# Performance work log

Measured on AMD Instinct MI355X. Metric: run time of the kernel, lower is better.

## Reference

```python
import jax, jax.numpy as jnp
import numpy as np

N = 4096          # total ensemble boxes per frame
M = 20            # MAX_MERGE_NUMS
H = 16            # MergeNet hidden_c
COND_THRES = 0.2
IOU_THRES = 0.3


def setup_inputs() -> dict:
    key = jax.random.key(0)
    ks = jax.random.split(key, 6)
    u = jax.random.uniform(ks[0], (N, 9), dtype=jnp.float32)
    # realistic lidar boxes: centers in a ~140x80x8m range, dims in [0.5, 4.5), heading in [-pi, pi)
    centers = (u[:, 0:3] - 0.5) * jnp.array([140.0, 80.0, 8.0], jnp.float32)
    dims = u[:, 3:6] * 4.0 + 0.5
    heading = (u[:, 6:7] - 0.5) * (2.0 * np.pi)
    extra = u[:, 7:9]  # extra box attrs (cols 7:9), untouched by merge
    pred_boxes = jnp.concatenate([centers, dims, heading, extra], axis=-1)
    pred_scores = jax.random.uniform(ks[1], (N,), dtype=jnp.float32)
    pred_labels = jax.random.randint(ks[2], (N,), 0, 3)
    w1 = (jax.random.normal(ks[3], (M, H), jnp.float32) / np.sqrt(M)).astype(jnp.float32)
    b1 = jnp.zeros((H,), jnp.float32)
    w2 = (jax.random.normal(ks[4], (H, H), jnp.float32) / np.sqrt(H)).astype(jnp.float32)
    b2 = jnp.zeros((H,), jnp.float32)
    w3 = (jax.random.normal(ks[5], (H, 1), jnp.float32) / np.sqrt(H)).astype(jnp.float32)
    b3 = jnp.zeros((1,), jnp.float32)
    return dict(pred_boxes=pred_boxes, pred_scores=pred_scores, pred_labels=pred_labels,
                w1=w1, b1=b1, w2=w2, b2=b2, w3=w3, b3=b3)


def _bev_aligned(b):
    # boxes3d_lidar_to_aligned_bev_boxes: swap dx/dy when |limit_period(heading)| >= pi/4
    ang = b[..., 6] - jnp.floor(b[..., 6] / np.pi + 0.5) * np.pi
    swap = jnp.abs(ang) >= (np.pi / 4)
    dx = jnp.where(swap, b[..., 4], b[..., 3])
    dy = jnp.where(swap, b[..., 3], b[..., 4])
    return jnp.stack([b[..., 0] - dx / 2, b[..., 1] - dy / 2,
                      b[..., 0] + dx / 2, b[..., 1] + dy / 2], axis=-1)


def _iou_one_many(a, b):
    # axis-aligned BEV IoU of one box a[4] vs many b[N,4]
    xmin = jnp.maximum(a[0], b[:, 0]); ymin = jnp.maximum(a[1], b[:, 1])
    xmax = jnp.minimum(a[2], b[:, 2]); ymax = jnp.minimum(a[3], b[:, 3])
    inter = jnp.maximum(xmax - xmin, 0.0) * jnp.maximum(ymax - ymin, 0.0)
    area_a = (a[2] - a[0]) * (a[3] - a[1])
    area_b = (b[:, 2] - b[:, 0]) * (b[:, 3] - b[:, 1])
    return inter / jnp.maximum(area_a + area_b - inter, 1e-6)


def _nms_merge(pred_boxes, pred_scores, pred_labels, w1, b1, w2, b2, w3, b3):
    valid = pred_scores > COND_THRES
    sort_key = jnp.where(valid, pred_scores, -jnp.inf)
    order = jnp.argsort(-sort_key)                 # descending by score; invalid sink
    boxes9 = pred_boxes[order]
    labels = pred_labels[order]
    scores = pred_scores[order]
    suppressed0 = ~valid[order]
    boxes7 = boxes9[:, :7]
    bev0 = _bev_aligned(boxes7)                    # merged boxes get suppressed, so bev is static

    def mergenet(ob):                              # ob: [M, 7] -> merged box [7]
        x = ob.T                                   # [7, M] (k is the feature axis)
        h = jax.nn.relu(x @ w1 + b1)
        h = jax.nn.relu(h @ w2 + b2)
        return (h @ w3 + b3)[:, 0]

    def step(suppressed, i):
        active = ~suppressed[i]
        same = (labels == labels[i]) & (~suppressed)
        iou = _iou_one_many(bev0[i], bev0)         # [N]
        over = (iou > IOU_THRES) & same            # includes self (iou=1)
        count = jnp.sum(over)
        rank = jnp.cumsum(over) - 1                # slot of each overlap, in score order
        tgt = jnp.where(over & (rank < M), rank, M)
        ob = jnp.zeros((M, 7), boxes7.dtype).at[tgt].set(boxes7, mode='drop')
        bi = boxes7[i]
        new_box = jnp.where(count > 1, mergenet(ob), bi)
        new_box = new_box.at[3:6].set(jnp.maximum(new_box[3:6], 1e-5))
        out_box = jnp.where(active, new_box, bi)
        return suppressed | (over & active), (out_box, active)

    _, (merged7, keep) = jax.lax.scan(step, suppressed0, jnp.arange(N))
    out_boxes = jnp.concatenate([merged7, boxes9[:, 7:9]], axis=-1)   # [N, 9]
    return out_boxes, scores, labels, keep


def reference(pred_boxes, pred_scores, pred_labels, w1, b1, w2, b2, w3, b3):
    # Returns fixed-shape (boxes9, scores, labels, keep_mask); rows with keep=False
    # correspond to boxes that torch's dynamic version would have removed.
    return _nms_merge(pred_boxes, pred_scores, pred_labels, w1, b1, w2, b2, w3, b3)
```

## Files before the change

kernel.cpp:

```cpp
#include <hip/hip_runtime.h>
#include <cstdint>

typedef unsigned long long u64;
typedef unsigned int u32;

#define NB 4096
#define NW 64
#define MM 20
#define HH 16
#define COND_THRES 0.2f
#define IOU_THRES 0.3f
#define PI_F  3.14159265358979323846f
#define PI4_F 0.78539816339744830962f

#define WS_KEPT    0
#define WS_MASK    32768
#define WS_BOX9S   (WS_MASK + NB*NW*8)
#define WS_BEVS    (WS_BOX9S + NB*9*4)
#define WS_SCORES  (WS_BEVS + NB*16)
#define WS_LABELS  (WS_SCORES + NB*4)
#define WS_SUPSTEP (WS_LABELS + NB*4)
#define WS_NBRW    (WS_SUPSTEP + NB*4)
#define WS_PART    (WS_NBRW + NB*8)

__device__ __forceinline__ u64 sort_key(float s, int i) {
  u32 sb = (s > COND_THRES) ? __float_as_uint(s) : 0u;
  return ((u64)(sb ^ 0xFFFFFFFFu) << 12) | (u64)i;
}

__global__ void __launch_bounds__(256) k_rank(const float* __restrict__ scores,
                                              u32* __restrict__ partial,
                                              u64* __restrict__ nbrw) {
  __shared__ u64 kj[256];
  int tid = threadIdx.x;
  int j = blockIdx.y * 256 + tid;
  kj[tid] = sort_key(scores[j], j);
  __syncthreads();
  int i = blockIdx.x * 256 + tid;
  if (blockIdx.y == 0) nbrw[i] = 0;
  u64 ki = sort_key(scores[i], i);
  int cnt = 0;
  #pragma unroll 16
  for (int t = 0; t < 256; ++t) cnt += (kj[t] < ki) ? 1 : 0;
  partial[i * 16 + blockIdx.y] = (u32)cnt;
}

__global__ void __launch_bounds__(256) k_scatter(const u32* __restrict__ partial,
                                                 const float* __restrict__ scores,
                                                 const float* __restrict__ boxes9,
                                                 const int* __restrict__ labels,
                                                 float* __restrict__ box9s, float4* __restrict__ bevs,
                                                 float* __restrict__ scoress, int* __restrict__ labelss) {
  #pragma clang fp contract(off)
  int i = blockIdx.x * 256 + threadIdx.x;
  const uint4* p4 = (const uint4*)(partial + i * 16);
  uint4 a0 = p4[0], a1 = p4[1], a2 = p4[2], a3 = p4[3];
  int r = (int)(a0.x + a0.y + a0.z + a0.w + a1.x + a1.y + a1.z + a1.w +
                a2.x + a2.y + a2.z + a2.w + a3.x + a3.y + a3.z + a3.w);
  float b[9];
  #pragma unroll
  for (int f = 0; f < 9; ++f) b[f] = boxes9[i * 9 + f];
  #pragma unroll
  for (int f = 0; f < 9; ++f) box9s[r * 9 + f] = b[f];
  float ang = b[6] - floorf(b[6] / PI_F + 0.5f) * PI_F;
  bool sw = fabsf(ang) >= PI4_F;
  float dx = sw ? b[4] : b[3];
  float dy = sw ? b[3] : b[4];
  bevs[r] = make_float4(b[0] - dx * 0.5f, b[1] - dy * 0.5f,
                        b[0] + dx * 0.5f, b[1] + dy * 0.5f);
  scoress[r] = scores[i];
  labelss[r] = labels[i];
}

__global__ void __launch_bounds__(64) k_mask(const float4* __restrict__ bevs,
                                             const int* __restrict__ labelss,
                                             const float* __restrict__ scoress,
                                             u64* __restrict__ mask,
                                             u64* __restrict__ nbrw) {
  #pragma clang fp contract(off)
  __shared__ float4 bj[64];
  __shared__ int lj[64];
  int t = threadIdx.x;
  int jt = blockIdx.x;
  int it = blockIdx.y;
  int j = jt * 64 + t;
  bj[t] = bevs[j];
  lj[t] = labelss[j];
  u64 vj = __ballot(scoress[j] > COND_THRES);
  int i = it * 64 + t;
  float4 a = bevs[i];
  int la = labelss[i];
  float area_a = (a.z - a.x) * (a.w - a.y);
  __syncthreads();
  u64 w = 0;
  #pragma unroll 8
  for (int kk = 0; kk < 64; ++kk) {
    float4 bb = bj[kk];
    float xmin = fmaxf(a.x, bb.x), ymin = fmaxf(a.y, bb.y);
    float xmax = fminf(a.z, bb.z), ymax = fminf(a.w, bb.w);
    float inter = fmaxf(xmax - xmin, 0.0f) * fmaxf(ymax - ymin, 0.0f);
    float area_b = (bb.z - bb.x) * (bb.w - bb.y);
    float iou = inter / fmaxf(area_a + area_b - inter, 1e-6f);
    if ((iou > IOU_THRES) && (la == lj[kk])) w |= (1ull << kk);
  }
  mask[(u64)i * NW + jt] = w;
  if (jt <= it) {
    u64 below = (jt < it) ? ~0ull : ((1ull << t) - 1ull);
    if (w & vj & below) atomicOr(&nbrw[i], 1ull << jt);
  }
}

__global__ void __launch_bounds__(1024) k_nms(const u64* __restrict__ mask,
                                              const u64* __restrict__ nbrw,
                                              const float* __restrict__ scoress,
                                              u64* __restrict__ keptOut) {
  __shared__ u64 decided[64], kept[64];
  __shared__ int remaining;
  int tid = threadIdx.x;
  if (tid < 64) {
    u64 v = 0;
    #pragma unroll 8
    for (int b = 0; b < 64; ++b)
      if (scoress[(tid << 6) | b] > COND_THRES) v |= (1ull << b);
    decided[tid] = ~v;
    kept[tid] = 0;
  }
  if (tid == 0) remaining = 0;
  __syncthreads();
  if (tid < 64) atomicAdd(&remaining, __popcll(~decided[tid]));
  u64 cw0[4], cw1[4];
  u32 meta[4];
  #pragma unroll
  for (int s = 0; s < 4; ++s) {
    int i = tid + (s << 10);
    int wi = i >> 6;
    u64 bit = 1ull << (i & 63);
    u64 t = nbrw[i];
    int n = 0; u32 ovf = 0;
    u64 c0 = 0, c1 = 0; u32 i0 = 0, i1 = 0;
    while (t) {
      int w = __builtin_ctzll(t);
      t &= t - 1;
      u64 below = (w < wi) ? ~0ull : (bit - 1ull);
      u64 m = mask[(u64)i * NW + w] & below;
      if (n == 0)      { c0 = m; i0 = (u32)w; }
      else if (n == 1) { c1 = m; i1 = (u32)w; }
      else ovf = 1;
      ++n;
    }
    cw0[s] = c0; cw1[s] = c1;
    meta[s] = i0 | (i1 << 6) | ((u32)(n > 2 ? 2 : n) << 12) | (ovf << 14);
  }
  __syncthreads();
  while (remaining > 0) {
    int decIdx[4]; bool decKept[4]; int nDec = 0;
    #pragma unroll
    for (int s = 0; s < 4; ++s) {
      int i = tid + (s << 10);
      int wi = i >> 6;
      u64 bit = 1ull << (i & 63);
      if (decided[wi] & bit) continue;
      bool hasU = false, hasK = false;
      u32 mt = meta[s];
      if (!(mt & (1u << 14))) {
        int n = (mt >> 12) & 3;
        if (n >= 1) {
          int w = mt & 63;
          hasU = hasU || ((cw0[s] & ~decided[w]) != 0ull);
          hasK = hasK || ((cw0[s] & kept[w]) != 0ull);
        }
        if (n >= 2) {
          int w = (mt >> 6) & 63;
          hasU = hasU || ((cw1[s] & ~decided[w]) != 0ull);
          hasK = hasK || ((cw1[s] & kept[w]) != 0ull);
        }
      } else {
        u64 t = nbrw[i];
        while (t) {
          int w = __builtin_ctzll(t);
          t &= t - 1;
          u64 below = (w < wi) ? ~0ull : (bit - 1ull);
          u64 m = mask[(u64)i * NW + w] & below;
          hasU = hasU || ((m & ~decided[w]) != 0ull);
          hasK = hasK || ((m & kept[w]) != 0ull);
        }
      }
      if (!hasU) { decIdx[nDec] = i; decKept[nDec] = !hasK; ++nDec; }
    }
    __syncthreads();
    for (int d = 0; d < nDec; ++d) {
      int i = decIdx[d];
      u64 bit = 1ull << (i & 63);
      atomicOr(&decided[i >> 6], bit);
      if (decKept[d]) atomicOr(&kept[i >> 6], bit);
      atomicSub(&remaining, 1);
    }
    __syncthreads();
  }
  if (tid < 64) keptOut[tid] = kept[tid];
}

__global__ void __launch_bounds__(256) k_supstep(const u64* __restrict__ mask,
                                                 const u64* __restrict__ kept,
                                                 const float* __restrict__ scoress,
                                                 int* __restrict__ supstep) {
  __shared__ u64 K[64];
  if (threadIdx.x < 64) K[threadIdx.x] = kept[threadIdx.x];
  __syncthreads();
  int j = blockIdx.x * 256 + threadIdx.x;
  if (!(scoress[j] > COND_THRES)) { supstep[j] = -1; return; }
  int res = 0x7FFFFFFF;
  #pragma unroll 4
  for (int w = 0; w < 64; ++w) {
    u64 m = mask[(u64)j * NW + w] & K[w];
    if (m) { res = (w << 6) + __builtin_ctzll(m); break; }
  }
  supstep[j] = res;
}

__global__ void __launch_bounds__(64) k_merge(
    const u64* __restrict__ mask, const int* __restrict__ supstep,
    const float* __restrict__ box9s, const float* __restrict__ scoress,
    const int* __restrict__ labelss,
    const float* __restrict__ w1, const float* __restrict__ b1,
    const float* __restrict__ w2, const float* __restrict__ b2,
    const float* __restrict__ w3, const float* __restrict__ b3,
    float* __restrict__ out) {
  #pragma clang fp contract(off)
  __shared__ int candList[MM];
  __shared__ float ob[MM][7];
  __shared__ float h1[7][HH];
  __shared__ float h2[7][HH];
  __shared__ float res[7];
  int i = blockIdx.x;
  int t = threadIdx.x;
  bool active = (supstep[i] == i);
  u64 wq = 0;
  int cnt = 0;
  if (active) {
    u64 w = mask[(u64)i * NW + t];
    while (w) {
      int b = __builtin_ctzll(w);
      w &= w - 1;
      int j = (t << 6) | b;
      if (supstep[j] >= i) { wq |= (1ull << b); cnt++; }
    }
  }
  int incl = cnt;
  #pragma unroll
  for (int off = 1; off < 64; off <<= 1) {
    int v = __shfl_up(incl, off);
    if (t >= off) incl += v;
  }
  int excl = incl - cnt;
  int count = __shfl(incl, 63);
  bool merged = active && (count > 1);
  if (merged && wq) {
    int pos = excl;
    u64 ww = wq;
    while (ww && pos < MM) {
      int b = __builtin_ctzll(ww);
      ww &= ww - 1;
      candList[pos++] = (t << 6) | b;
    }
  }
  __syncthreads();
  if (merged) {
    int nc = count < MM ? count : MM;
    if (t < MM) {
      if (t < nc) {
        int j = candList[t];
        #pragma unroll
        for (int f = 0; f < 7; ++f) ob[t][f] = box9s[j * 9 + f];
      } else {
        #pragma unroll
        for (int f = 0; f < 7; ++f) ob[t][f] = 0.0f;
      }
    }
    __syncthreads();
    for (int o = t; o < 7 * HH; o += 64) {
      int f = o >> 4, hh = o & 15;
      float acc = b1[hh];
      #pragma unroll
      for (int m = 0; m < MM; ++m) acc += ob[m][f] * w1[m * HH + hh];
      h1[f][hh] = fmaxf(acc, 0.0f);
    }
    __syncthreads();
    for (int o = t; o < 7 * HH; o += 64) {
      int f = o >> 4, oo = o & 15;
      float acc = b2[oo];
      #pragma unroll
      for (int k = 0; k < HH; ++k) acc += h1[f][k] * w2[k * HH + oo];
      h2[f][oo] = fmaxf(acc, 0.0f);
    }
    __syncthreads();
    if (t < 7) {
      float acc = b3[0];
      #pragma unroll
      for (int k = 0; k < HH; ++k) acc += h2[t][k] * w3[k];
      if (t >= 3 && t < 6) acc = fmaxf(acc, 1e-5f);
      res[t] = acc;
    }
    __syncthreads();
  }
  if (t < 9) {
    float v = box9s[i * 9 + t];
    if (merged && t < 7) v = res[t];
    out[i * 9 + t] = v;
  }
  if (t == 0) {
    out[NB * 9 + i]          = scoress[i];
    out[NB * 9 + NB + i]     = (float)labelss[i];
    out[NB * 9 + 2 * NB + i] = active ? 1.0f : 0.0f;
  }
}

extern "C" void kernel_launch(void* const* d_in, const int* in_sizes, int n_in,
                              void* d_out, int out_size, void* d_ws, size_t ws_size,
                              hipStream_t stream) {
  const float* boxes9 = (const float*)d_in[0];
  const float* scores = (const float*)d_in[1];
  const int*   labels = (const int*)d_in[2];
  const float* w1 = (const float*)d_in[3];
  const float* b1 = (const float*)d_in[4];
  const float* w2 = (const float*)d_in[5];
  const float* b2 = (const float*)d_in[6];
  const float* w3 = (const float*)d_in[7];
  const float* b3 = (const float*)d_in[8];
  char* ws = (char*)d_ws;
  u64*    kept    = (u64*)(ws + WS_KEPT);
  u64*    mask    = (u64*)(ws + WS_MASK);
  float*  box9s   = (float*)(ws + WS_BOX9S);
  float4* bevs    = (float4*)(ws + WS_BEVS);
  float*  scoress = (float*)(ws + WS_SCORES);
  int*    labelss = (int*)(ws + WS_LABELS);
  int*    supstep = (int*)(ws + WS_SUPSTEP);
  u64*    nbrw    = (u64*)(ws + WS_NBRW);
  u32*    part    = (u32*)(ws + WS_PART);
  float*  out     = (float*)d_out;

  hipLaunchKernelGGL(k_rank,    dim3(16, 16),   dim3(256),  0, stream, scores, part, nbrw);
  hipLaunchKernelGGL(k_scatter, dim3(NB / 256), dim3(256),  0, stream, part, scores, boxes9, labels,
                     box9s, bevs, scoress, labelss);
  hipLaunchKernelGGL(k_mask,    dim3(64, 64),   dim3(64),   0, stream, bevs, labelss, scoress,
                     mask, nbrw);
  hipLaunchKernelGGL(k_nms,     dim3(1),        dim3(1024), 0, stream, mask, nbrw, scoress, kept);
  hipLaunchKernelGGL(k_supstep, dim3(NB / 256), dim3(256),  0, stream, mask, kept, scoress, supstep);
  hipLaunchKernelGGL(k_merge,   dim3(NB),       dim3(64),   0, stream, mask, supstep,
                     box9s, scoress, labelss, w1, b1, w2, b2, w3, b3, out);
}
```

Before: 132.7 us.

## Fuse rank and scatter kernels; drop supstep pass by recomputing suppression in merge

Merges the score-ranking and scatter kernels into one k_sort kernel. In it, each group of 16 threads counts one element's rank over all tiles, reduces the count with shuffles, and writes the sorted box data. This removes the partial-count buffer. The k_supstep kernel is also removed: k_merge now takes kept and valid bitmasks and, for each active box, checks whether each overlapping candidate is suppressed by an earlier kept box by scanning its mask rows. This saves two launches and intermediate round-trips, but adds a per-candidate scan of mask words inside k_merge that could be costly for late boxes.

```diff
diff --git a/kernel.cpp b/kernel.cpp
--- a/kernel.cpp
+++ b/kernel.cpp
@@ -14,62 +14,63 @@
 #define PI4_F 0.78539816339744830962f
 
 #define WS_KEPT    0
+#define WS_VALID   512
 #define WS_MASK    32768
 #define WS_BOX9S   (WS_MASK + NB*NW*8)
 #define WS_BEVS    (WS_BOX9S + NB*9*4)
 #define WS_SCORES  (WS_BEVS + NB*16)
 #define WS_LABELS  (WS_SCORES + NB*4)
-#define WS_SUPSTEP (WS_LABELS + NB*4)
-#define WS_NBRW    (WS_SUPSTEP + NB*4)
-#define WS_PART    (WS_NBRW + NB*8)
+#define WS_NBRW    (WS_LABELS + NB*4)
 
 __device__ __forceinline__ u64 sort_key(float s, int i) {
   u32 sb = (s > COND_THRES) ? __float_as_uint(s) : 0u;
   return ((u64)(sb ^ 0xFFFFFFFFu) << 12) | (u64)i;
 }
 
-__global__ void __launch_bounds__(256) k_rank(const float* __restrict__ scores,
-                                              u32* __restrict__ partial,
+__global__ void __launch_bounds__(256) k_sort(const float* __restrict__ scores,
+                                              const float* __restrict__ boxes9,
+                                              const int* __restrict__ labels,
+                                              float* __restrict__ box9s, float4* __restrict__ bevs,
+                                              float* __restrict__ scoress, int* __restrict__ labelss,
                                               u64* __restrict__ nbrw) {
+  #pragma clang fp contract(off)
   __shared__ u64 kj[256];
   int tid = threadIdx.x;
-  int j = blockIdx.y * 256 + tid;
-  kj[tid] = sort_key(scores[j], j);
-  __syncthreads();
-  int i = blockIdx.x * 256 + tid;
-  if (blockIdx.y == 0) nbrw[i] = 0;
+  int il = tid >> 4;
+  int sub = tid & 15;
+  int i = blockIdx.x * 16 + il;
+  if (blockIdx.x * 256 + tid < NB) nbrw[blockIdx.x * 256 + tid] = 0;
+  if (blockIdx.x < 16) nbrw[blockIdx.x * 256 + tid] = 0;
   u64 ki = sort_key(scores[i], i);
   int cnt = 0;
-  #pragma unroll 16
-  for (int t = 0; t < 256; ++t) cnt += (kj[t] < ki) ? 1 : 0;
-  partial[i * 16 + blockIdx.y] = (u32)cnt;
-}
-
-__global__ void __launch_bounds__(256) k_scatter(const u32* __restrict__ partial,
-                                                 const float* __restrict__ scores,
-                                                 const float* __restrict__ boxes9,
-                                                 const int* __restrict__ labels,
-                                                 float* __restrict__ box9s, float4* __restrict__ bevs,
-                                                 float* __restrict__ scoress, int* __restrict__ labelss) {
-  #pragma clang fp contract(off)
-  int i = blockIdx.x * 256 + threadIdx.x;
-  const uint4* p4 = (const uint4*)(partial + i * 16);
-  uint4 a0 = p4[0], a1 = p4[1], a2 = p4[2], a3 = p4[3];
-  int r = (int)(a0.x + a0.y + a0.z + a0.w + a1.x + a1.y + a1.z + a1.w +
-                a2.x + a2.y + a2.z + a2.w + a3.x + a3.y + a3.z + a3.w);
-  float b[9];
+  for (int tile = 0; tile < 16; ++tile) {
+    __syncthreads();
+    int j = tile * 256 + tid;
+    kj[tid] = sort_key(scores[j], j);
+    __syncthreads();
+    #pragma unroll
+    for (int q = 0; q < 16; ++q)
+      cnt += (kj[q * 16 + sub] < ki) ? 1 : 0;
+  }
   #pragma unroll
-  for (int f = 0; f < 9; ++f) b[f] = boxes9[i * 9 + f];
-  #pragma unroll
-  for (int f = 0; f < 9; ++f) box9s[r * 9 + f] = b[f];
-  float ang = b[6] - floorf(b[6] / PI_F + 0.5f) * PI_F;
-  bool sw = fabsf(ang) >= PI4_F;
-  float dx = sw ? b[4] : b[3];
-  float dy = sw ? b[3] : b[4];
-  bevs[r] = make_float4(b[0] - dx * 0.5f, b[1] - dy * 0.5f,
-                        b[0] + dx * 0.5f, b[1] + dy * 0.5f);
-  scoress[r] = scores[i];
-  labelss[r] = labels[i];
+  for (int off = 8; off >= 1; off >>= 1)
+    cnt += __shfl_down(cnt, off, 16);
+  if (sub == 0) {
+    int r = cnt;
+    float b[9];
+    #pragma unroll
+    for (int f = 0; f < 9; ++f) b[f] = boxes9[i * 9 + f];
+    #pragma unroll
+    for (int f = 0; f < 9; ++f) box9s[r * 9 + f] = b[f];
+    float ang = b[6] - floorf(b[6] / PI_F + 0.5f) * PI_F;
+    bool sw = fabsf(ang) >= PI4_F;
+    float dx = sw ? b[4] : b[3];
+    float dy = sw ? b[3] : b[4];
+    bevs[r] = make_float4(b[0] - dx * 0.5f, b[1] - dy * 0.5f,
+                          b[0] + dx * 0.5f, b[1] + dy * 0.5f);
+    scoress[r] = scores[i];
+    labelss[r] = labels[i];
+  }
 }
 
 __global__ void __launch_bounds__(64) k_mask(const float4* __restrict__ bevs,
@@ -113,7 +114,8 @@
 __global__ void __launch_bounds__(1024) k_nms(const u64* __restrict__ mask,
                                               const u64* __restrict__ nbrw,
                                               const float* __restrict__ scoress,
-                                              u64* __restrict__ keptOut) {
+                                              u64* __restrict__ keptOut,
+                                              u64* __restrict__ validOut) {
   __shared__ u64 decided[64], kept[64];
   __shared__ int remaining;
   int tid = threadIdx.x;
@@ -124,6 +126,7 @@
       if (scoress[(tid << 6) | b] > COND_THRES) v |= (1ull << b);
     decided[tid] = ~v;
     kept[tid] = 0;
+    validOut[tid] = v;
   }
   if (tid == 0) remaining = 0;
   __syncthreads();
@@ -200,26 +203,9 @@
   if (tid < 64) keptOut[tid] = kept[tid];
 }
 
-__global__ void __launch_bounds__(256) k_supstep(const u64* __restrict__ mask,
-                                                 const u64* __restrict__ kept,
-                                                 const float* __restrict__ scoress,
-                                                 int* __restrict__ supstep) {
-  __shared__ u64 K[64];
-  if (threadIdx.x < 64) K[threadIdx.x] = kept[threadIdx.x];
-  __syncthreads();
-  int j = blockIdx.x * 256 + threadIdx.x;
-  if (!(scoress[j] > COND_THRES)) { supstep[j] = -1; return; }
-  int res = 0x7FFFFFFF;
-  #pragma unroll 4
-  for (int w = 0; w < 64; ++w) {
-    u64 m = mask[(u64)j * NW + w] & K[w];
-    if (m) { res = (w << 6) + __builtin_ctzll(m); break; }
-  }
-  supstep[j] = res;
-}
-
 __global__ void __launch_bounds__(64) k_merge(
-    const u64* __restrict__ mask, const int* __restrict__ supstep,
+    const u64* __restrict__ mask, const u64* __restrict__ keptIn,
+    const u64* __restrict__ validIn,
     const float* __restrict__ box9s, const float* __restrict__ scoress,
     const int* __restrict__ labelss,
     const float* __restrict__ w1, const float* __restrict__ b1,
@@ -227,6 +213,7 @@
     const float* __restrict__ w3, const float* __restrict__ b3,
     float* __restrict__ out) {
   #pragma clang fp contract(off)
+  __shared__ u64 Ksh[64];
   __shared__ int candList[MM];
   __shared__ float ob[MM][7];
   __shared__ float h1[7][HH];
@@ -234,16 +221,27 @@
   __shared__ float res[7];
   int i = blockIdx.x;
   int t = threadIdx.x;
-  bool active = (supstep[i] == i);
+  Ksh[t] = keptIn[t];
+  u64 vw = validIn[t];
+  __syncthreads();
+  const int wi = i >> 6;
+  bool active = ((Ksh[wi] >> (i & 63)) & 1ull) != 0ull;
   u64 wq = 0;
   int cnt = 0;
   if (active) {
-    u64 w = mask[(u64)i * NW + t];
+    u64 w = mask[(u64)i * NW + t] & vw;
+    const u64 topmask = (1ull << (i & 63)) - 1ull;
     while (w) {
       int b = __builtin_ctzll(w);
       w &= w - 1;
       int j = (t << 6) | b;
-      if (supstep[j] >= i) { wq |= (1ull << b); cnt++; }
+      bool sb = false;
+      for (int w2 = 0; w2 <= wi; ++w2) {
+        u64 kk = Ksh[w2];
+        if (w2 == wi) kk &= topmask;
+        sb = sb || ((mask[(u64)j * NW + w2] & kk) != 0ull);
+      }
+      if (!sb) { wq |= (1ull << b); cnt++; }
     }
   }
   int incl = cnt;
@@ -329,23 +327,21 @@
   const float* b3 = (const float*)d_in[8];
   char* ws = (char*)d_ws;
   u64*    kept    = (u64*)(ws + WS_KEPT);
+  u64*    valid   = (u64*)(ws + WS_VALID);
   u64*    mask    = (u64*)(ws + WS_MASK);
   float*  box9s   = (float*)(ws + WS_BOX9S);
   float4* bevs    = (float4*)(ws + WS_BEVS);
   float*  scoress = (float*)(ws + WS_SCORES);
   int*    labelss = (int*)(ws + WS_LABELS);
-  int*    supstep = (int*)(ws + WS_SUPSTEP);
   u64*    nbrw    = (u64*)(ws + WS_NBRW);
-  u32*    part    = (u32*)(ws + WS_PART);
   float*  out     = (float*)d_out;
 
-  hipLaunchKernelGGL(k_rank,    dim3(16, 16),   dim3(256),  0, stream, scores, part, nbrw);
-  hipLaunchKernelGGL(k_scatter, dim3(NB / 256), dim3(256),  0, stream, part, scores, boxes9, labels,
-                     box9s, bevs, scoress, labelss);
-  hipLaunchKernelGGL(k_mask,    dim3(64, 64),   dim3(64),   0, stream, bevs, labelss, scoress,
+  hipLaunchKernelGGL(k_sort,  dim3(NB / 16), dim3(256),  0, stream, scores, boxes9, labels,
+                     box9s, bevs, scoress, labelss, nbrw);
+  hipLaunchKernelGGL(k_mask,  dim3(64, 64),  dim3(64),   0, stream, bevs, labelss, scoress,
                      mask, nbrw);
-  hipLaunchKernelGGL(k_nms,     dim3(1),        dim3(1024), 0, stream, mask, nbrw, scoress, kept);
-  hipLaunchKernelGGL(k_supstep, dim3(NB / 256), dim3(256),  0, stream, mask, kept, scoress, supstep);
-  hipLaunchKernelGGL(k_merge,   dim3(NB),       dim3(64),   0, stream, mask, supstep,
+  hipLaunchKernelGGL(k_nms,   dim3(1),       dim3(1024), 0, stream, mask, nbrw, scoress,
+                     kept, valid);
+  hipLaunchKernelGGL(k_merge, dim3(NB),      dim3(64),   0, stream, mask, kept, valid,
                      box9s, scoress, labelss, w1, b1, w2, b2, w3, b3, out);
 }
```

Result: slower. 137.2 us (+3.3%).

## Fuse rank and scatter kernels into a single sort kernel

Applied to the files above, without the earlier changes.

Merges the rank-counting kernel and the scatter kernel into one. Each block now handles 16 boxes, with 16 threads per box splitting the 4096 comparisons, and reduces the counts with a segmented shuffle before scattering. This removes one launch and the global partial-count buffer round trip. In exchange each block streams all 4096 keys through shared memory in 16 tiles, which adds barriers and redundant loads across 256 blocks.

```diff
diff --git a/kernel.cpp b/kernel.cpp
--- a/kernel.cpp
+++ b/kernel.cpp
@@ -21,55 +21,55 @@
 #define WS_LABELS  (WS_SCORES + NB*4)
 #define WS_SUPSTEP (WS_LABELS + NB*4)
 #define WS_NBRW    (WS_SUPSTEP + NB*4)
-#define WS_PART    (WS_NBRW + NB*8)
 
 __device__ __forceinline__ u64 sort_key(float s, int i) {
   u32 sb = (s > COND_THRES) ? __float_as_uint(s) : 0u;
   return ((u64)(sb ^ 0xFFFFFFFFu) << 12) | (u64)i;
 }
 
-__global__ void __launch_bounds__(256) k_rank(const float* __restrict__ scores,
-                                              u32* __restrict__ partial,
+__global__ void __launch_bounds__(256) k_sort(const float* __restrict__ scores,
+                                              const float* __restrict__ boxes9,
+                                              const int* __restrict__ labels,
+                                              float* __restrict__ box9s, float4* __restrict__ bevs,
+                                              float* __restrict__ scoress, int* __restrict__ labelss,
                                               u64* __restrict__ nbrw) {
+  #pragma clang fp contract(off)
   __shared__ u64 kj[256];
   int tid = threadIdx.x;
-  int j = blockIdx.y * 256 + tid;
-  kj[tid] = sort_key(scores[j], j);
-  __syncthreads();
-  int i = blockIdx.x * 256 + tid;
-  if (blockIdx.y == 0) nbrw[i] = 0;
+  int il = tid >> 4;
+  int sub = tid & 15;
+  int i = blockIdx.x * 16 + il;
+  if (blockIdx.x < 16) nbrw[blockIdx.x * 256 + tid] = 0;
   u64 ki = sort_key(scores[i], i);
   int cnt = 0;
-  #pragma unroll 16
-  for (int t = 0; t < 256; ++t) cnt += (kj[t] < ki) ? 1 : 0;
-  partial[i * 16 + blockIdx.y] = (u32)cnt;
-}
-
-__global__ void __launch_bounds__(256) k_scatter(const u32* __restrict__ partial,
-                                                 const float* __restrict__ scores,
-                                                 const float* __restrict__ boxes9,
-                                                 const int* __restrict__ labels,
-                                                 float* __restrict__ box9s, float4* __restrict__ bevs,
-                                                 float* __restrict__ scoress, int* __restrict__ labelss) {
-  #pragma clang fp contract(off)
-  int i = blockIdx.x * 256 + threadIdx.x;
-  const uint4* p4 = (const uint4*)(partial + i * 16);
-  uint4 a0 = p4[0], a1 = p4[1], a2 = p4[2], a3 = p4[3];
-  int r = (int)(a0.x + a0.y + a0.z + a0.w + a1.x + a1.y + a1.z + a1.w +
-                a2.x + a2.y + a2.z + a2.w + a3.x + a3.y + a3.z + a3.w);
-  float b[9];
+  for (int tile = 0; tile < 16; ++tile) {
+    __syncthreads();
+    int j = tile * 256 + tid;
+    kj[tid] = sort_key(scores[j], j);
+    __syncthreads();
+    #pragma unroll
+    for (int q = 0; q < 16; ++q)
+      cnt += (kj[q * 16 + sub] < ki) ? 1 : 0;
+  }
   #pragma unroll
-  for (int f = 0; f < 9; ++f) b[f] = boxes9[i * 9 + f];
-  #pragma unroll
-  for (int f = 0; f < 9; ++f) box9s[r * 9 + f] = b[f];
-  float ang = b[6] - floorf(b[6] / PI_F + 0.5f) * PI_F;
-  bool sw = fabsf(ang) >= PI4_F;
-  float dx = sw ? b[4] : b[3];
-  float dy = sw ? b[3] : b[4];
-  bevs[r] = make_float4(b[0] - dx * 0.5f, b[1] - dy * 0.5f,
-                        b[0] + dx * 0.5f, b[1] + dy * 0.5f);
-  scoress[r] = scores[i];
-  labelss[r] = labels[i];
+  for (int off = 8; off >= 1; off >>= 1)
+    cnt += __shfl_down(cnt, off, 16);
+  if (sub == 0) {
+    int r = cnt;
+    float b[9];
+    #pragma unroll
+    for (int f = 0; f < 9; ++f) b[f] = boxes9[i * 9 + f];
+    #pragma unroll
+    for (int f = 0; f < 9; ++f) box9s[r * 9 + f] = b[f];
+    float ang = b[6] - floorf(b[6] / PI_F + 0.5f) * PI_F;
+    bool sw = fabsf(ang) >= PI4_F;
+    float dx = sw ? b[4] : b[3];
+    float dy = sw ? b[3] : b[4];
+    bevs[r] = make_float4(b[0] - dx * 0.5f, b[1] - dy * 0.5f,
+                          b[0] + dx * 0.5f, b[1] + dy * 0.5f);
+    scoress[r] = scores[i];
+    labelss[r] = labels[i];
+  }
 }
 
 __global__ void __launch_bounds__(64) k_mask(const float4* __restrict__ bevs,
@@ -336,12 +336,10 @@
   int*    labelss = (int*)(ws + WS_LABELS);
   int*    supstep = (int*)(ws + WS_SUPSTEP);
   u64*    nbrw    = (u64*)(ws + WS_NBRW);
-  u32*    part    = (u32*)(ws + WS_PART);
   float*  out     = (float*)d_out;
 
-  hipLaunchKernelGGL(k_rank,    dim3(16, 16),   dim3(256),  0, stream, scores, part, nbrw);
-  hipLaunchKernelGGL(k_scatter, dim3(NB / 256), dim3(256),  0, stream, part, scores, boxes9, labels,
-                     box9s, bevs, scoress, labelss);
+  hipLaunchKernelGGL(k_sort,    dim3(NB / 16),  dim3(256),  0, stream, scores, boxes9, labels,
+                     box9s, bevs, scoress, labelss, nbrw);
   hipLaunchKernelGGL(k_mask,    dim3(64, 64),   dim3(64),   0, stream, bevs, labelss, scoress,
                      mask, nbrw);
   hipLaunchKernelGGL(k_nms,     dim3(1),        dim3(1024), 0, stream, mask, nbrw, scoress, kept);
```

After: 136.5 us. 2.9% more time.
